# Kernel tuning notes

Hardware: AMD Instinct MI355X
Metric: run time of the kernel (lower is better)

The kernel has to match this reference:

```python
import jax, jax.numpy as jnp
import numpy as np
from jax import lax

N = 56          # markers (graph nodes)
C_IN, C1, C2 = 3, 32, 64   # marker_gcn_dim = [3, 32, 64]
B, T = 32, 64   # batch, window
H = 512         # lstm hidden
OUT = 256       # output_num


def _adjacency():
    """Chain skeleton + random extra edges, symmetrized, with self loops
    (mirrors dense_to_sparse + add_self_loops on a connectivity matrix)."""
    rng = np.random.RandomState(0)
    A = np.zeros((N, N), np.float32)
    for i in range(N - 1):
        A[i, i + 1] = 1.0
    for _ in range(2 * N):
        a, b = rng.randint(0, N, 2)
        A[a, b] = 1.0
    A = np.maximum(A, A.T)
    np.fill_diagonal(A, 1.0)
    return A


def _block_mask(out_c, in_c, A):
    # mask[out_c*tgt:(tgt+1)*out_c, in_c*src:(src+1)*in_c] = 1 iff edge (src->tgt)
    return jnp.asarray(np.kron(A, np.ones((out_c, in_c), np.float32)))


def setup_inputs() -> dict:
    key = jax.random.key(0)
    ks = jax.random.split(key, 16)
    A = _adjacency()

    def w(k, shape, fan_in):
        return jax.random.normal(k, shape, jnp.float32) / np.sqrt(fan_in)

    d1_in, d1_out = C_IN * N, C1 * N      # 168, 1792
    d2_in, d2_out = C1 * N, C2 * N        # 1792, 3584
    lstm_in = C2 * N                      # 3584

    inp = {
        "x": jax.random.normal(ks[0], (B, T, d1_in), jnp.float32),
        "w1": w(ks[1], (d1_out, d1_in), d1_in),
        "b1": w(ks[2], (d1_out,), d1_in),
        "mask1": _block_mask(C1, C_IN, A),
        "w2": w(ks[3], (d2_out, d2_in), d2_in),
        "b2": w(ks[4], (d2_out,), d2_in),
        "mask2": _block_mask(C2, C1, A),
        "w_ih_f": w(ks[5], (4 * H, lstm_in), lstm_in),
        "w_hh_f": w(ks[6], (4 * H, H), H),
        "b_ih_f": w(ks[7], (4 * H,), H),
        "b_hh_f": w(ks[8], (4 * H,), H),
        "w_ih_b": w(ks[9], (4 * H, lstm_in), lstm_in),
        "w_hh_b": w(ks[10], (4 * H, H), H),
        "b_ih_b": w(ks[11], (4 * H,), H),
        "b_hh_b": w(ks[12], (4 * H,), H),
        "wo1": w(ks[13], (OUT, 2 * H), 2 * H),
        "bo1": jnp.zeros((OUT,), jnp.float32),
        "wo2": w(ks[14], (OUT, OUT), OUT),
        "bo2": jnp.zeros((OUT,), jnp.float32),
    }
    return inp


def _lstm_dir(xt, w_ih, w_hh, b, h0, c0):
    # xt: [T, B, I]; PyTorch gate order: i, f, g, o
    x_proj = jnp.einsum('tbi,gi->tbg', xt, w_ih) + b  # precompute input GEMM

    def step(carry, xp):
        h, c = carry
        g = xp + h @ w_hh.T
        i, f, gg, o = jnp.split(g, 4, axis=-1)
        c = jax.nn.sigmoid(f) * c + jax.nn.sigmoid(i) * jnp.tanh(gg)
        h = jax.nn.sigmoid(o) * jnp.tanh(c)
        return (h, c), h

    (h, c), ys = lax.scan(step, (h0, c0), x_proj)
    return ys, h, c


def _forward(x, w1, b1, mask1, w2, b2, mask2,
             w_ih_f, w_hh_f, b_ih_f, b_hh_f,
             w_ih_b, w_hh_b, b_ih_b, b_hh_b,
             wo1, bo1, wo2, bo2):
    bt = B * T
    h = x.reshape(bt, -1)
    # SkeletonLinear 1 + ReLU (edge-masked GEMM)
    h = jax.nn.relu(h @ (w1 * mask1).T + b1)
    # SkeletonLinear 2 + ReLU
    h = jax.nn.relu(h @ (w2 * mask2).T + b2)
    seq = h.reshape(B, T, -1).transpose(1, 0, 2)  # [T, B, 3584]

    h0 = jnp.zeros((B, H), x.dtype)
    c0 = jnp.zeros((B, H), x.dtype)
    yf, hf, cf = _lstm_dir(seq, w_ih_f, w_hh_f, b_ih_f + b_hh_f, h0, c0)
    yb, hb, cb = _lstm_dir(seq[::-1], w_ih_b, w_hh_b, b_ih_b + b_hh_b, h0, c0)
    y = jnp.concatenate([yf, yb[::-1]], axis=-1)  # [T, B, 2H]
    y = y.transpose(1, 0, 2).reshape(bt, 2 * H)

    # Dropout(0.5) is identity in eval mode
    o = jax.nn.relu(y @ wo1.T + bo1)
    o = o @ wo2.T + bo2
    out = o.reshape(B, T, OUT)
    hidden = jnp.stack([hf, hb])  # [2, B, H]
    c = jnp.stack([cf, cb])
    return out, hidden, c


def reference(x, w1, b1, mask1, w2, b2, mask2,
              w_ih_f, w_hh_f, b_ih_f, b_hh_f,
              w_ih_b, w_hh_b, b_ih_b, b_hh_b,
              wo1, bo1, wo2, bo2):
    return _forward(x, w1, b1, mask1, w2, b2, mask2,
                    w_ih_f, w_hh_f, b_ih_f, b_hh_f,
                    w_ih_b, w_hh_b, b_ih_b, b_hh_b,
                    wo1, bo1, wo2, bo2)
```

## Files before the change

kernel.cpp:

```cpp
#include <hip/hip_runtime.h>
#include <stddef.h>

typedef float f32x4 __attribute__((ext_vector_type(4)));
typedef short s16x8 __attribute__((ext_vector_type(8)));

__device__ __forceinline__ short f2bf(float f) {
    unsigned u = __float_as_uint(f);
    unsigned r = (u + 0x7fffu + ((u >> 16) & 1u)) >> 16;
    return (short)r;
}

__device__ __forceinline__ void load_lds16(const void* g, void* l) {
    __builtin_amdgcn_global_load_lds(
        (const __attribute__((address_space(1))) unsigned int*)g,
        (__attribute__((address_space(3))) unsigned int*)l, 16, 0, 0);
}

template<bool OBF16, bool RELU>
__global__ __launch_bounds__(256)
void gemm_mfma(const short* __restrict__ A, const short* __restrict__ W,
               const float* __restrict__ bias, void* __restrict__ Cv,
               int M, int N, int K)
{
    __shared__ short As[128 * 64];
    __shared__ short Bs[128 * 64];
    const int tid = threadIdx.x;
    const int l    = tid & 63;
    const int wave = tid >> 6;
    const int wr = wave >> 1, wc = wave & 1;

    const int nwg = gridDim.x * gridDim.y;
    int flat = blockIdx.y * gridDim.x + blockIdx.x;
    flat = (flat & 7) * (nwg >> 3) + (flat >> 3);
    const int n0 = (flat % gridDim.x) * 128;
    const int m0 = (flat / gridDim.x) * 128;

    f32x4 acc[4][4];
#pragma unroll
    for (int i = 0; i < 4; ++i)
#pragma unroll
        for (int j = 0; j < 4; ++j) {
            acc[i][j][0] = 0.f; acc[i][j][1] = 0.f;
            acc[i][j][2] = 0.f; acc[i][j][3] = 0.f;
        }

    const int srow = tid >> 3;
    const int gc   = (tid & 7) ^ (srow & 7);
    const short* gA = A + (size_t)(m0 + srow) * K + gc * 8;
    const short* gB = W + (size_t)(n0 + srow) * K + gc * 8;
    char* AsB = (char*)As;
    char* BsB = (char*)Bs;
    char* dstA = AsB + wave * 1024;
    char* dstB = BsB + wave * 1024;

    int aoff[4], boff[4], soff[2];
#pragma unroll
    for (int mi = 0; mi < 4; ++mi) aoff[mi] = (wr * 64 + mi * 16 + (l & 15)) * 128;
#pragma unroll
    for (int ni = 0; ni < 4; ++ni) boff[ni] = (wc * 64 + ni * 16 + (l & 15)) * 128;
#pragma unroll
    for (int kh = 0; kh < 2; ++kh) soff[kh] = ((kh * 4 + (l >> 4)) ^ (l & 7)) * 16;

    for (int kt = 0; kt < K; kt += 64) {
#pragma unroll
        for (int j = 0; j < 4; ++j) {
            load_lds16(gA + (size_t)j * 32 * K + kt, dstA + j * 4096);
            load_lds16(gB + (size_t)j * 32 * K + kt, dstB + j * 4096);
        }
        __syncthreads();
#pragma unroll
        for (int kh = 0; kh < 2; ++kh) {
            s16x8 af[4], bfr[4];
#pragma unroll
            for (int mi = 0; mi < 4; ++mi)
                af[mi] = *(const s16x8*)(AsB + aoff[mi] + soff[kh]);
#pragma unroll
            for (int ni = 0; ni < 4; ++ni)
                bfr[ni] = *(const s16x8*)(BsB + boff[ni] + soff[kh]);
#pragma unroll
            for (int mi = 0; mi < 4; ++mi)
#pragma unroll
                for (int ni = 0; ni < 4; ++ni)
                    acc[mi][ni] = __builtin_amdgcn_mfma_f32_16x16x32_bf16(
                        af[mi], bfr[ni], acc[mi][ni], 0, 0, 0);
        }
        __syncthreads();
    }

    const int colf = l & 15, rowf = (l >> 4) * 4;
#pragma unroll
    for (int mi = 0; mi < 4; ++mi)
#pragma unroll
        for (int ni = 0; ni < 4; ++ni) {
            const int n = n0 + wc * 64 + ni * 16 + colf;
            const float bv = bias[n];
#pragma unroll
            for (int r = 0; r < 4; ++r) {
                const int m = m0 + wr * 64 + mi * 16 + rowf + r;
                float v = acc[mi][ni][r] + bv;
                if (RELU) v = fmaxf(v, 0.f);
                if (OBF16) ((short*)Cv)[(size_t)m * N + n] = f2bf(v);
                else       ((float*)Cv)[(size_t)m * N + n] = v;
            }
        }
}

__global__ void conv_bf16(const float* __restrict__ in, const float* __restrict__ mask,
                          short* __restrict__ out, int n4)
{
    int i = blockIdx.x * blockDim.x + threadIdx.x;
    if (i >= n4) return;
    float4 v = ((const float4*)in)[i];
    if (mask) {
        float4 m = ((const float4*)mask)[i];
        v.x *= m.x; v.y *= m.y; v.z *= m.z; v.w *= m.w;
    }
    short4 o;
    o.x = f2bf(v.x); o.y = f2bf(v.y); o.z = f2bf(v.z); o.w = f2bf(v.w);
    ((short4*)out)[i] = o;
}

__global__ void padconv_bf16(const float* __restrict__ in, const float* __restrict__ mask,
                             short* __restrict__ out, int M, int Kin4, int Kout4)
{
    int idx = blockIdx.x * blockDim.x + threadIdx.x;
    if (idx >= M * Kout4) return;
    int m = idx / Kout4, k4 = idx % Kout4;
    float4 v = make_float4(0.f, 0.f, 0.f, 0.f);
    if (k4 < Kin4) {
        v = ((const float4*)in)[(size_t)m * Kin4 + k4];
        if (mask) {
            float4 mm = ((const float4*)mask)[(size_t)m * Kin4 + k4];
            v.x *= mm.x; v.y *= mm.y; v.z *= mm.z; v.w *= mm.w;
        }
    }
    short4 o;
    o.x = f2bf(v.x); o.y = f2bf(v.y); o.z = f2bf(v.z); o.w = f2bf(v.w);
    ((short4*)out)[(size_t)m * Kout4 + k4] = o;
}

__global__ void bias_sum_kernel(const float* __restrict__ bihf, const float* __restrict__ bhhf,
                                const float* __restrict__ bihb, const float* __restrict__ bhhb,
                                float* __restrict__ o)
{
    int i = blockIdx.x * blockDim.x + threadIdx.x;
    if (i < 2048)      o[i] = bihf[i] + bhhf[i];
    else if (i < 4096) o[i] = bihb[i - 2048] + bhhb[i - 2048];
}

__global__ __launch_bounds__(256, 2)
void lstm_step2(int t,
                const float* __restrict__ xp,
                const short* __restrict__ whb,
                short* __restrict__ hbuf,
                float* __restrict__ cbuf,
                short* __restrict__ y,
                float* __restrict__ out)
{
    __shared__ short wT[8 * 32 * 64];
    __shared__ short hT[8 * 32 * 64];
    __shared__ float gbuf[4][32][9];

    const int bid = blockIdx.x;
    const int dir = bid >> 6;
    const int jg  = bid & 63;
    const int j0  = jg * 8;
    const int tid = threadIdx.x;
    const int l    = tid & 63;
    const int wave = tid >> 6;
    const int tt = dir ? (63 - t) : t;

    const short* whh = whb + (size_t)dir * 1048576;
    const short* hread  = hbuf + dir * 2 * 16384 + (t & 1) * 16384;
    short*       hwrite = hbuf + dir * 2 * 16384 + ((t + 1) & 1) * 16384;
    float*       cst    = cbuf + dir * 16384;

    char* wTB = (char*)wT;
    char* hTB = (char*)hT;

    const int gb = tid >> 3;
    const int gj = tid & 7;
    const int j  = j0 + gj;

    const float* xpr = xp + ((size_t)(gb * 64 + tt)) * 4096 + dir * 2048 + j;
    const float xi = xpr[0], xf = xpr[512], xg = xpr[1024], xo = xpr[1536];
    float c_old = cst[gb * 512 + j];

    const int rloc = wave * 8 + (l >> 3);
    const int gc   = (l & 7) ^ (rloc & 7);
    const short* gW = whh + (size_t)((rloc >> 3) * 512 + j0 + (rloc & 7)) * 512 + gc * 8;
    const short* gH = hread + rloc * 512 + gc * 8;
    char* dstW = wTB + wave * 1024;
    char* dstH = hTB + wave * 1024;

#pragma unroll
    for (int kt = 0; kt < 8; ++kt) {
        load_lds16(gH + kt * 64, dstH + kt * 4096);
        load_lds16(gW + kt * 64, dstW + kt * 4096);
    }

    int soff[2];
    soff[0] = ((0 * 4 + (l >> 4)) ^ (l & 7)) * 16;
    soff[1] = ((1 * 4 + (l >> 4)) ^ (l & 7)) * 16;
    const int a0off = (l & 15) * 128;
    const int a1off = (16 + (l & 15)) * 128;
    const int bof   = (wave * 8 + (l & 7)) * 128;

    __syncthreads();

    f32x4 acc0, acc1;
    acc0[0] = 0.f; acc0[1] = 0.f; acc0[2] = 0.f; acc0[3] = 0.f;
    acc1 = acc0;
#pragma unroll
    for (int kt = 0; kt < 8; ++kt) {
#pragma unroll
        for (int kh = 0; kh < 2; ++kh) {
            s16x8 bv = *(const s16x8*)(wTB + kt * 4096 + bof + soff[kh]);
            s16x8 a0 = *(const s16x8*)(hTB + kt * 4096 + a0off + soff[kh]);
            s16x8 a1 = *(const s16x8*)(hTB + kt * 4096 + a1off + soff[kh]);
            acc0 = __builtin_amdgcn_mfma_f32_16x16x32_bf16(a0, bv, acc0, 0, 0, 0);
            acc1 = __builtin_amdgcn_mfma_f32_16x16x32_bf16(a1, bv, acc1, 0, 0, 0);
        }
    }

    if ((l & 15) < 8) {
        const int sj = l & 15, r4 = (l >> 4) * 4;
#pragma unroll
        for (int r = 0; r < 4; ++r) {
            gbuf[wave][r4 + r][sj]      = acc0[r];
            gbuf[wave][16 + r4 + r][sj] = acc1[r];
        }
    }
    __syncthreads();

    {
        float g_i = gbuf[0][gb][gj] + xi;
        float g_f = gbuf[1][gb][gj] + xf;
        float g_g = gbuf[2][gb][gj] + xg;
        float g_o = gbuf[3][gb][gj] + xo;
        float si = 1.f / (1.f + expf(-g_i));
        float sf = 1.f / (1.f + expf(-g_f));
        float so = 1.f / (1.f + expf(-g_o));
        float tg = tanhf(g_g);
        float c_new = sf * c_old + si * tg;
        float h_new = so * tanhf(c_new);

        cst[gb * 512 + j] = c_new;
        const short hb16 = f2bf(h_new);
        hwrite[gb * 512 + j] = hb16;
        y[((size_t)(gb * 64 + tt)) * 1024 + dir * 512 + j] = hb16;

        if (t == 63) {
            out[524288 + dir * 16384 + gb * 512 + j]         = h_new;
            out[524288 + 32768 + dir * 16384 + gb * 512 + j] = c_new;
        }
    }
}

extern "C" void kernel_launch(void* const* d_in, const int* in_sizes, int n_in,
                              void* d_out, int out_size, void* d_ws, size_t ws_size,
                              hipStream_t stream)
{
    const float* x     = (const float*)d_in[0];
    const float* w1    = (const float*)d_in[1];
    const float* b1    = (const float*)d_in[2];
    const float* mask1 = (const float*)d_in[3];
    const float* w2    = (const float*)d_in[4];
    const float* b2    = (const float*)d_in[5];
    const float* mask2 = (const float*)d_in[6];
    const float* wihf  = (const float*)d_in[7];
    const float* whhf  = (const float*)d_in[8];
    const float* bihf  = (const float*)d_in[9];
    const float* bhhf  = (const float*)d_in[10];
    const float* wihb  = (const float*)d_in[11];
    const float* whhb  = (const float*)d_in[12];
    const float* bihb  = (const float*)d_in[13];
    const float* bhhb  = (const float*)d_in[14];
    const float* wo1   = (const float*)d_in[15];
    const float* bo1   = (const float*)d_in[16];
    const float* wo2   = (const float*)d_in[17];
    const float* bo2   = (const float*)d_in[18];
    float* out = (float*)d_out;

    char* base = (char*)d_ws;
    short* wqb  = (short*)base;
    short* whb  = (short*)base;
    char*  Breg = base + 29360128;
    short* h2b  = (short*)Breg;
    short* xpad = (short*)Breg;
    short* w1mb = (short*)(Breg + 786432);
    char*  Creg = base + 44040192;
    float* xp   = (float*)Creg;
    short* w2b  = (short*)Creg;
    char*  Dreg = base + 77594624;
    short* h1b  = (short*)Dreg;
    short* ybuf = (short*)Dreg;
    short* o1   = (short*)(Dreg + 4194304);
    short* wo1b = (short*)(Dreg + 5242880);
    short* wo2b = (short*)(Dreg + 5767168);
    char*  Ereg = base + 84934656;
    short* hbuf = (short*)Ereg;
    float* cbuf = (float*)(Ereg + 131072);
    float* bsum = (float*)(Ereg + 262144);

    hipMemsetAsync(Ereg, 0, 262144, stream);
    bias_sum_kernel<<<16, 256, 0, stream>>>(bihf, bhhf, bihb, bhhb, bsum);

    conv_bf16<<<6272, 256, 0, stream>>>(w2, mask2, w2b, 6422528 / 4);
    conv_bf16<<<7168, 256, 0, stream>>>(wihf, nullptr, wqb, 7340032 / 4);
    conv_bf16<<<7168, 256, 0, stream>>>(wihb, nullptr, wqb + 7340032, 7340032 / 4);
    padconv_bf16<<<384, 256, 0, stream>>>(x, nullptr, xpad, 2048, 42, 48);
    padconv_bf16<<<336, 256, 0, stream>>>(w1, mask1, w1mb, 1792, 42, 48);

    gemm_mfma<true, true><<<dim3(1792 / 128, 2048 / 128), 256, 0, stream>>>(
        xpad, w1mb, b1, h1b, 2048, 1792, 192);

    gemm_mfma<true, true><<<dim3(3584 / 128, 2048 / 128), 256, 0, stream>>>(
        h1b, w2b, b2, h2b, 2048, 3584, 1792);

    gemm_mfma<false, false><<<dim3(4096 / 128, 2048 / 128), 256, 0, stream>>>(
        h2b, wqb, bsum, xp, 2048, 4096, 3584);

    conv_bf16<<<1024, 256, 0, stream>>>(whhf, nullptr, whb, 1048576 / 4);
    conv_bf16<<<1024, 256, 0, stream>>>(whhb, nullptr, whb + 1048576, 1048576 / 4);
    conv_bf16<<<256, 256, 0, stream>>>(wo1, nullptr, wo1b, 262144 / 4);
    conv_bf16<<<64, 256, 0, stream>>>(wo2, nullptr, wo2b, 65536 / 4);

    for (int t = 0; t < 64; ++t)
        lstm_step2<<<128, 256, 0, stream>>>(t, xp, whb, hbuf, cbuf, ybuf, out);

    gemm_mfma<true, true><<<dim3(256 / 128, 2048 / 128), 256, 0, stream>>>(
        ybuf, wo1b, bo1, o1, 2048, 256, 1024);
    gemm_mfma<false, false><<<dim3(256 / 128, 2048 / 128), 256, 0, stream>>>(
        o1, wo2b, bo2, out, 2048, 256, 256);
}
```

Baseline: 613.8 us.

## Load LSTM recurrent MFMA operands directly from global and remap GEMM tile order

The per-timestep LSTM kernel no longer stages W_hh and h through LDS with async global-to-LDS loads and a barrier. Each lane now reads its MFMA fragments straight from global memory, which removes the LDS round trip and one __syncthreads from the latency-bound recurrent step. The cost is uncoalesced 16-byte reads that depend on cache hits. Separately, the GEMM workgroup rank is now walked column-major, changing which tiles run together for L2 reuse.

```diff
diff --git a/kernel.cpp b/kernel.cpp
--- a/kernel.cpp
+++ b/kernel.cpp
@@ -30,10 +30,10 @@
     const int wr = wave >> 1, wc = wave & 1;
 
     const int nwg = gridDim.x * gridDim.y;
-    int flat = blockIdx.y * gridDim.x + blockIdx.x;
-    flat = (flat & 7) * (nwg >> 3) + (flat >> 3);
-    const int n0 = (flat % gridDim.x) * 128;
-    const int m0 = (flat / gridDim.x) * 128;
+    const int f = blockIdx.y * gridDim.x + blockIdx.x;
+    const int rank = (f & 7) * (nwg >> 3) + (f >> 3);
+    const int n0 = (rank / gridDim.y) * 128;
+    const int m0 = (rank % gridDim.y) * 128;
 
     f32x4 acc[4][4];
 #pragma unroll
@@ -148,8 +148,8 @@
     else if (i < 4096) o[i] = bihb[i - 2048] + bhhb[i - 2048];
 }
 
-__global__ __launch_bounds__(256, 2)
-void lstm_step2(int t,
+__global__ __launch_bounds__(256)
+void lstm_step3(int t,
                 const float* __restrict__ xp,
                 const short* __restrict__ whb,
                 short* __restrict__ hbuf,
@@ -157,8 +157,6 @@
                 short* __restrict__ y,
                 float* __restrict__ out)
 {
-    __shared__ short wT[8 * 32 * 64];
-    __shared__ short hT[8 * 32 * 64];
     __shared__ float gbuf[4][32][9];
 
     const int bid = blockIdx.x;
@@ -170,14 +168,11 @@
     const int wave = tid >> 6;
     const int tt = dir ? (63 - t) : t;
 
-    const short* whh = whb + (size_t)dir * 1048576;
+    const short* whh    = whb + (size_t)dir * 1048576;
     const short* hread  = hbuf + dir * 2 * 16384 + (t & 1) * 16384;
     short*       hwrite = hbuf + dir * 2 * 16384 + ((t + 1) & 1) * 16384;
     float*       cst    = cbuf + dir * 16384;
 
-    char* wTB = (char*)wT;
-    char* hTB = (char*)hT;
-
     const int gb = tid >> 3;
     const int gj = tid & 7;
     const int j  = j0 + gj;
@@ -186,49 +181,30 @@
     const float xi = xpr[0], xf = xpr[512], xg = xpr[1024], xo = xpr[1536];
     float c_old = cst[gb * 512 + j];
 
-    const int rloc = wave * 8 + (l >> 3);
-    const int gc   = (l & 7) ^ (rloc & 7);
-    const short* gW = whh + (size_t)((rloc >> 3) * 512 + j0 + (rloc & 7)) * 512 + gc * 8;
-    const short* gH = hread + rloc * 512 + gc * 8;
-    char* dstW = wTB + wave * 1024;
-    char* dstH = hTB + wave * 1024;
-
-#pragma unroll
-    for (int kt = 0; kt < 8; ++kt) {
-        load_lds16(gH + kt * 64, dstH + kt * 4096);
-        load_lds16(gW + kt * 64, dstW + kt * 4096);
-    }
-
-    int soff[2];
-    soff[0] = ((0 * 4 + (l >> 4)) ^ (l & 7)) * 16;
-    soff[1] = ((1 * 4 + (l >> 4)) ^ (l & 7)) * 16;
-    const int a0off = (l & 15) * 128;
-    const int a1off = (16 + (l & 15)) * 128;
-    const int bof   = (wave * 8 + (l & 7)) * 128;
-
-    __syncthreads();
+    const int fc = l & 15;
+    const int kc = (l >> 4) * 8;
+    const short* pB  = whh + ((size_t)(wave * 512 + j0 + (fc & 7))) * 512 + kc;
+    const short* pA0 = hread + fc * 512 + kc;
+    const short* pA1 = hread + (16 + fc) * 512 + kc;
 
     f32x4 acc0, acc1;
     acc0[0] = 0.f; acc0[1] = 0.f; acc0[2] = 0.f; acc0[3] = 0.f;
     acc1 = acc0;
 #pragma unroll
-    for (int kt = 0; kt < 8; ++kt) {
-#pragma unroll
-        for (int kh = 0; kh < 2; ++kh) {
-            s16x8 bv = *(const s16x8*)(wTB + kt * 4096 + bof + soff[kh]);
-            s16x8 a0 = *(const s16x8*)(hTB + kt * 4096 + a0off + soff[kh]);
-            s16x8 a1 = *(const s16x8*)(hTB + kt * 4096 + a1off + soff[kh]);
-            acc0 = __builtin_amdgcn_mfma_f32_16x16x32_bf16(a0, bv, acc0, 0, 0, 0);
-            acc1 = __builtin_amdgcn_mfma_f32_16x16x32_bf16(a1, bv, acc1, 0, 0, 0);
-        }
-    }
-
-    if ((l & 15) < 8) {
-        const int sj = l & 15, r4 = (l >> 4) * 4;
+    for (int kt = 0; kt < 16; ++kt) {
+        s16x8 bv = *(const s16x8*)(pB  + kt * 32);
+        s16x8 a0 = *(const s16x8*)(pA0 + kt * 32);
+        s16x8 a1 = *(const s16x8*)(pA1 + kt * 32);
+        acc0 = __builtin_amdgcn_mfma_f32_16x16x32_bf16(a0, bv, acc0, 0, 0, 0);
+        acc1 = __builtin_amdgcn_mfma_f32_16x16x32_bf16(a1, bv, acc1, 0, 0, 0);
+    }
+
+    if (fc < 8) {
+        const int r4 = (l >> 4) * 4;
 #pragma unroll
         for (int r = 0; r < 4; ++r) {
-            gbuf[wave][r4 + r][sj]      = acc0[r];
-            gbuf[wave][16 + r4 + r][sj] = acc1[r];
+            gbuf[wave][r4 + r][fc]      = acc0[r];
+            gbuf[wave][16 + r4 + r][fc] = acc1[r];
         }
     }
     __syncthreads();
@@ -327,7 +303,7 @@
     conv_bf16<<<64, 256, 0, stream>>>(wo2, nullptr, wo2b, 65536 / 4);
 
     for (int t = 0; t < 64; ++t)
-        lstm_step2<<<128, 256, 0, stream>>>(t, xp, whb, hbuf, cbuf, ybuf, out);
+        lstm_step3<<<128, 256, 0, stream>>>(t, xp, whb, hbuf, cbuf, ybuf, out);
 
     gemm_mfma<true, true><<<dim3(256 / 128, 2048 / 128), 256, 0, stream>>>(
         ybuf, wo1b, bo1, o1, 2048, 256, 1024);
```

Result: slower. 843.0 us (+37.3%).
